# Kernel tuning notes

Measured on AMD Instinct MI355X. Metric: run time of the kernel, lower is better.

Reference implementation:

```python
import jax, jax.numpy as jnp
import numpy as np

NEG_INF = -9e15  # matches the torch source's large-negative mask value
LRELU_SLOPE = 0.2


def setup_inputs() -> dict:
    key = jax.random.key(0)
    k1, k2, k3, k4, k5, k6 = jax.random.split(key, 6)
    N, D_IN, D_OUT = 8192, 512, 256
    h = jax.random.normal(k1, (N, D_IN), dtype=jnp.float32)
    adj = jax.random.randint(k2, (N, N), 0, 2, dtype=jnp.int32)
    # xavier_uniform with gain=1.414 for W [out, in] and a [1, 2*out]
    lim_W = 1.414 * np.sqrt(6.0 / (D_IN + D_OUT))
    lim_a = 1.414 * np.sqrt(6.0 / (2 * D_OUT + 1))
    W_w = jax.random.uniform(k3, (D_OUT, D_IN), minval=-lim_W, maxval=lim_W, dtype=jnp.float32)
    W_b = jax.random.normal(k4, (D_OUT,), dtype=jnp.float32) * 0.01
    a_w = jax.random.uniform(k5, (1, 2 * D_OUT), minval=-lim_a, maxval=lim_a, dtype=jnp.float32)
    a_b = jax.random.normal(k6, (1,), dtype=jnp.float32) * 0.01
    return {"h": h, "adj": adj, "W_w": W_w, "W_b": W_b, "a_w": a_w, "a_b": a_b}


def reference(h, adj, W_w, W_b, a_w, a_b):
    # wh = W(h): [N, d_out]
    wh = h @ W_w.T + W_b
    d_out = wh.shape[-1]
    # a(cat([wh_i, wh_j])) decomposes: a_src . wh_i + a_dst . wh_j + a_b
    # (identical math to the O(N^2 * 2d) repeat/cat in the torch source)
    a_src, a_dst = a_w[0, :d_out], a_w[0, d_out:]
    s_src = wh @ a_src  # [N]
    s_dst = wh @ a_dst  # [N]
    e = jax.nn.leaky_relu(s_src[:, None] + s_dst[None, :] + a_b[0], LRELU_SLOPE)  # [N, N]
    masked = jnp.where(adj > 0, e, jnp.float32(NEG_INF))
    attn = jax.nn.softmax(masked, axis=1)  # softmax over neighbors j
    return attn @ wh  # [N, d_out]
```

## Files before the change

kernel.cpp:

```cpp
#include <hip/hip_runtime.h>

typedef unsigned short ushort_t;
typedef unsigned int uint_t;
typedef __attribute__((ext_vector_type(8))) short short8;
typedef __attribute__((ext_vector_type(4))) float f32x4;
typedef __attribute__((ext_vector_type(4))) int i32x4;
typedef __attribute__((ext_vector_type(4))) uint_t u32x4;
typedef __attribute__((ext_vector_type(4))) ushort_t u16x4;

#define LRELU_SLOPE 0.2f
#define LOG2E 1.44269504f

static __device__ __forceinline__ ushort_t f2bf(float f) {
    uint_t u = __builtin_bit_cast(uint_t, f);
    uint_t r = (u + 0x7fffu + ((u >> 16) & 1u)) >> 16;
    return (ushort_t)r;
}
static __device__ __forceinline__ uint4 pack8(float4 a, float4 b) {
    uint4 r;
    r.x = (uint_t)f2bf(a.x) | ((uint_t)f2bf(a.y) << 16);
    r.y = (uint_t)f2bf(a.z) | ((uint_t)f2bf(a.w) << 16);
    r.z = (uint_t)f2bf(b.x) | ((uint_t)f2bf(b.y) << 16);
    r.w = (uint_t)f2bf(b.z) | ((uint_t)f2bf(b.w) << 16);
    return r;
}
static __device__ __forceinline__ uint_t cvt_pk_bf16(float lo, float hi) {
    uint_t r;
    asm("v_cvt_pk_bf16_f32 %0, %1, %2" : "=v"(r) : "v"(lo), "v"(hi));
    return r;
}

__launch_bounds__(256, 2)
__global__ void k1_gemm(const float* __restrict__ h, const float* __restrict__ W,
                        const float* __restrict__ Wb, const float* __restrict__ aw,
                        ushort_t* __restrict__ whB, float* __restrict__ s_src,
                        float* __restrict__ s_dst) {
    __shared__ __align__(16) ushort_t aT[256 * 72];
    __shared__ __align__(16) ushort_t bT[32 * 72];
    __shared__ float redLds[2][4][32];

    const int t = threadIdx.x;
    const int wv = t >> 6, ln = t & 63;
    const int i0 = blockIdx.x * 32;
    const int srow = t >> 3, sch = t & 7;
    const int row0 = ln & 15, kq = ln >> 4;

    f32x4 acc[4][2];
#pragma unroll
    for (int mt = 0; mt < 4; ++mt)
#pragma unroll
        for (int nt = 0; nt < 2; ++nt) acc[mt][nt] = (f32x4){0.f, 0.f, 0.f, 0.f};

    for (int k0 = 0; k0 < 512; k0 += 64) {
        __syncthreads();
#pragma unroll
        for (int r = 0; r < 8; ++r) {
            const float* gp = W + (size_t)(r * 32 + srow) * 512 + k0 + sch * 8;
            float4 x0 = *(const float4*)gp;
            float4 x1 = *(const float4*)(gp + 4);
            *(uint4*)(aT + (r * 32 + srow) * 72 + sch * 8) = pack8(x0, x1);
        }
        {
            const float* gp = h + (size_t)(i0 + srow) * 512 + k0 + sch * 8;
            float4 x0 = *(const float4*)gp;
            float4 x1 = *(const float4*)(gp + 4);
            *(uint4*)(bT + srow * 72 + sch * 8) = pack8(x0, x1);
        }
        __syncthreads();
#pragma unroll
        for (int ks = 0; ks < 2; ++ks) {
            short8 b[2];
#pragma unroll
            for (int nt = 0; nt < 2; ++nt)
                b[nt] = *(const short8*)(bT + (nt * 16 + row0) * 72 + ks * 32 + kq * 8);
#pragma unroll
            for (int mt = 0; mt < 4; ++mt) {
                short8 a = *(const short8*)(aT + (wv * 64 + mt * 16 + row0) * 72 + ks * 32 + kq * 8);
#pragma unroll
                for (int nt = 0; nt < 2; ++nt)
                    acc[mt][nt] = __builtin_amdgcn_mfma_f32_16x16x32_bf16(a, b[nt], acc[mt][nt], 0, 0, 0);
            }
        }
    }

    float psrc[2] = {0.f, 0.f}, pdst[2] = {0.f, 0.f};
#pragma unroll
    for (int mt = 0; mt < 4; ++mt) {
#pragma unroll
        for (int r = 0; r < 4; ++r) {
            const int o = wv * 64 + mt * 16 + (ln >> 4) * 4 + r;
            const float wbv = Wb[o];
            const float as = aw[o];
            const float ad = aw[256 + o];
#pragma unroll
            for (int nt = 0; nt < 2; ++nt) {
                const float v = acc[mt][nt][r] + wbv;
                psrc[nt] += v * as;
                pdst[nt] += v * ad;
                const int i = i0 + nt * 16 + (ln & 15);
                const int jt = i >> 6;
                const int khi = (i >> 5) & 1;
                const int kqi = (i >> 3) & 3;
                whB[((size_t)(jt * 2 + khi) * 256 + o) * 32 + kqi * 8 + (i & 7)] = f2bf(v);
            }
        }
    }
#pragma unroll
    for (int off = 16; off < 64; off <<= 1) {
#pragma unroll
        for (int nt = 0; nt < 2; ++nt) {
            psrc[nt] += __shfl_xor(psrc[nt], off, 64);
            pdst[nt] += __shfl_xor(pdst[nt], off, 64);
        }
    }
    if (ln < 16) {
#pragma unroll
        for (int nt = 0; nt < 2; ++nt) {
            redLds[0][wv][nt * 16 + ln] = psrc[nt];
            redLds[1][wv][nt * 16 + ln] = pdst[nt];
        }
    }
    __syncthreads();
    if (t < 32) {
        float s = 0.f;
#pragma unroll
        for (int w = 0; w < 4; ++w) s += redLds[0][w][t];
        s_src[i0 + t] = s * LOG2E;
    } else if (t < 64) {
        float s = 0.f;
#pragma unroll
        for (int w = 0; w < 4; ++w) s += redLds[1][w][t - 32];
        s_dst[i0 + t - 32] = s * LOG2E;
    }
}

__launch_bounds__(512, 2)
__global__ void k2_attn(const int* __restrict__ adj, const ushort_t* __restrict__ whB,
                        const float* __restrict__ s_src, const float* __restrict__ s_dst,
                        const float* __restrict__ ab_p, float* __restrict__ out0,
                        float* __restrict__ out1, float* __restrict__ zp, int jsplit) {
    __shared__ __align__(16) char smem[66560 + 256];
    ushort_t* pbuf = (ushort_t*)smem;
    float* exch = (float*)smem;
    float* zLds = (float*)(smem + 66560);

    const int t = threadIdx.x;
    const int wv = t >> 6, ln = t & 63;
    const int dq = wv & 3, kh = wv >> 2;
    const int row0 = ln & 15, kq = ln >> 4;
    const int split2 = (jsplit == 2);
    const int jb = split2 ? (int)(blockIdx.x & 1) : 0;
    const int ib = split2 ? (int)(blockIdx.x >> 1) : (int)blockIdx.x;
    const int i0 = ib * 64;
    const int jlen = split2 ? 4096 : 8192;
    const int jbase = jb * jlen;
    const int iters = jlen >> 6;
    const int prow = t >> 4, pjc = t & 15;

    const float ab = ab_p[0] * LOG2E;
    const float ssa0 = s_src[i0 + prow] + ab;
    const float ssa1 = s_src[i0 + 32 + prow] + ab;

    const int* aBase0 = adj + (size_t)(i0 + prow) * 8192 + jbase + pjc * 4;
    const int* aBase1 = aBase0 + (size_t)32 * 8192;
    const float* sBase = s_dst + jbase + pjc * 4;
    const ushort_t* bBase = whB + ((size_t)(jbase >> 6) * 2 + kh) * 8192
                            + (dq * 64 + row0) * 32 + kq * 8;

    f32x4 acc[4][4];
#pragma unroll
    for (int mt = 0; mt < 4; ++mt)
#pragma unroll
        for (int nt = 0; nt < 4; ++nt) acc[mt][nt] = (f32x4){0.f, 0.f, 0.f, 0.f};
    float zacc0 = 0.f, zacc1 = 0.f;

    i32x4 Av0 = __builtin_nontemporal_load((const i32x4*)aBase0);
    i32x4 Av1 = __builtin_nontemporal_load((const i32x4*)aBase1);
    f32x4 Sv = *(const f32x4*)sBase;
    short8 Bv[4];
#pragma unroll
    for (int nt = 0; nt < 4; ++nt) Bv[nt] = *(const short8*)(bBase + nt * 512);

#pragma unroll 2
    for (int it = 0; it < iters; ++it) {
        const int itn = (it < iters - 1) ? it + 1 : it;
        i32x4 Ac0 = Av0, Ac1 = Av1;
        f32x4 Sc = Sv;
        short8 Bc[4];
#pragma unroll
        for (int nt = 0; nt < 4; ++nt) Bc[nt] = Bv[nt];
        Av0 = __builtin_nontemporal_load((const i32x4*)(aBase0 + itn * 64));
        Av1 = __builtin_nontemporal_load((const i32x4*)(aBase1 + itn * 64));
        Sv = *(const f32x4*)(sBase + itn * 64);
        {
            const ushort_t* bN = bBase + (size_t)itn * 16384;
#pragma unroll
            for (int nt = 0; nt < 4; ++nt) Bv[nt] = *(const short8*)(bN + nt * 512);
        }

        {
            ushort_t* pc = pbuf + (it & 1) * 4608;
            float p[4];
            float z4 = 0.f;
#pragma unroll
            for (int k = 0; k < 4; ++k) {
                float sc = ssa0 + Sc[k];
                sc = fmaxf(sc, LRELU_SLOPE * sc);
                sc = fminf(sc, 86.562f);
                float pv = (Ac0[k] > 0) ? __builtin_amdgcn_exp2f(sc) : 0.f;
                z4 += pv;
                p[k] = pv;
            }
            zacc0 += z4;
            uint2 w0;
            w0.x = cvt_pk_bf16(p[0], p[1]);
            w0.y = cvt_pk_bf16(p[2], p[3]);
            *(uint2*)(pc + prow * 72 + pjc * 4) = w0;
            z4 = 0.f;
#pragma unroll
            for (int k = 0; k < 4; ++k) {
                float sc = ssa1 + Sc[k];
                sc = fmaxf(sc, LRELU_SLOPE * sc);
                sc = fminf(sc, 86.562f);
                float pv = (Ac1[k] > 0) ? __builtin_amdgcn_exp2f(sc) : 0.f;
                z4 += pv;
                p[k] = pv;
            }
            zacc1 += z4;
            uint2 w1;
            w1.x = cvt_pk_bf16(p[0], p[1]);
            w1.y = cvt_pk_bf16(p[2], p[3]);
            *(uint2*)(pc + (32 + prow) * 72 + pjc * 4) = w1;
        }
        __syncthreads();
        {
            const ushort_t* pc = pbuf + (it & 1) * 4608;
#pragma unroll
            for (int mt = 0; mt < 4; ++mt) {
                short8 a = *(const short8*)(pc + (mt * 16 + row0) * 72 + kh * 32 + kq * 8);
#pragma unroll
                for (int nt = 0; nt < 4; ++nt)
                    acc[mt][nt] = __builtin_amdgcn_mfma_f32_16x16x32_bf16(a, Bc[nt], acc[mt][nt], 0, 0, 0);
            }
        }
    }

    zacc0 += __shfl_xor(zacc0, 1, 64);
    zacc1 += __shfl_xor(zacc1, 1, 64);
    zacc0 += __shfl_xor(zacc0, 2, 64);
    zacc1 += __shfl_xor(zacc1, 2, 64);
    zacc0 += __shfl_xor(zacc0, 4, 64);
    zacc1 += __shfl_xor(zacc1, 4, 64);
    zacc0 += __shfl_xor(zacc0, 8, 64);
    zacc1 += __shfl_xor(zacc1, 8, 64);
    if ((t & 15) == 0) {
        if (split2) {
            zp[(size_t)jb * 8192 + i0 + prow] = zacc0;
            zp[(size_t)jb * 8192 + i0 + 32 + prow] = zacc1;
        } else {
            zLds[prow] = 1.0f / fmaxf(zacc0, 1e-30f);
            zLds[32 + prow] = 1.0f / fmaxf(zacc1, 1e-30f);
        }
    }

    __syncthreads();
    if (kh == 1) {
        float* p = exch + (dq * 64 + ln) * 65;
#pragma unroll
        for (int mt = 0; mt < 4; ++mt)
#pragma unroll
            for (int nt = 0; nt < 4; ++nt)
#pragma unroll
                for (int r = 0; r < 4; ++r) p[mt * 16 + nt * 4 + r] = acc[mt][nt][r];
    }
    __syncthreads();
    if (kh == 0) {
        float* outp = (jb == 0) ? out0 : out1;
        const float* p = exch + (dq * 64 + ln) * 65;
#pragma unroll
        for (int mt = 0; mt < 4; ++mt)
#pragma unroll
            for (int nt = 0; nt < 4; ++nt)
#pragma unroll
                for (int r = 0; r < 4; ++r) {
                    const int il = mt * 16 + (ln >> 4) * 4 + r;
                    const int d = dq * 64 + nt * 16 + (ln & 15);
                    const float v = acc[mt][nt][r] + p[mt * 16 + nt * 4 + r];
                    if (split2)
                        outp[(size_t)(i0 + il) * 256 + d] = v;
                    else
                        outp[(size_t)(i0 + il) * 256 + d] = v * zLds[il];
                }
    }
}

__global__ void k3_norm(float* __restrict__ out, const float* __restrict__ part,
                        const float* __restrict__ zp) {
    const int i = blockIdx.x, t = threadIdx.x;
    const float rz = 1.0f / fmaxf(zp[i] + zp[8192 + i], 1e-30f);
    const size_t idx = (size_t)i * 256 + t;
    out[idx] = (out[idx] + part[idx]) * rz;
}

extern "C" void kernel_launch(void* const* d_in, const int* in_sizes, int n_in, void* d_out,
                              int out_size, void* d_ws, size_t ws_size, hipStream_t stream) {
    int order[16];
    for (int i = 0; i < n_in; ++i) order[i] = i;
    for (int a = 0; a < n_in; ++a)
        for (int b = a + 1; b < n_in; ++b)
            if (in_sizes[order[b]] < in_sizes[order[a]]) {
                int tmp = order[a]; order[a] = order[b]; order[b] = tmp;
            }
    const float* ab = (const float*)d_in[order[0]];
    const float* Wb = (const float*)d_in[order[1]];
    const float* aw = (const float*)d_in[order[2]];
    const float* Ww = (const float*)d_in[order[3]];
    const float* h = (const float*)d_in[order[4]];
    const int* adj = (const int*)d_in[order[5]];

    char* ws = (char*)d_ws;
    ushort_t* whB = (ushort_t*)ws;
    float* ssrc = (float*)(ws + 4194304);
    float* sdst = (float*)(ws + 4227072);
    float* part = (float*)(ws + 4259840);
    float* zp = (float*)(ws + 12648448);
    const size_t need = 12713984;
    const int jsplit = (ws_size >= need) ? 2 : 1;

    hipLaunchKernelGGL(k1_gemm, dim3(256), dim3(256), 0, stream, h, Ww, Wb, aw, whB, ssrc, sdst);
    hipLaunchKernelGGL(k2_attn, dim3(128 * jsplit), dim3(512), 0, stream, adj, whB, ssrc, sdst,
                       ab, (float*)d_out, part, zp, jsplit);
    if (jsplit == 2)
        hipLaunchKernelGGL(k3_norm, dim3(8192), dim3(256), 0, stream, (float*)d_out, part, zp);
}
```

Before: 420.1 us.

## Fuse split-K normalization into attention kernel via last-arriver atomic flag

Removes the separate k3_norm launch. Each of the two j-split blocks writes its partial output and row sums to workspace, then increments a per-row-tile atomic counter. The block that arrives second reads the other block's partial and writes the final normalized output. The counters are reset inside k1_gemm. Software bf16 rounding is also replaced with the hardware v_cvt_pk_bf16 instruction. The cost is a larger workspace, an extra round of partial writes and reads, and reliance on correct fence/atomic ordering.

```diff
diff --git a/kernel.cpp b/kernel.cpp
--- a/kernel.cpp
+++ b/kernel.cpp
@@ -11,30 +11,28 @@
 #define LRELU_SLOPE 0.2f
 #define LOG2E 1.44269504f
 
-static __device__ __forceinline__ ushort_t f2bf(float f) {
-    uint_t u = __builtin_bit_cast(uint_t, f);
-    uint_t r = (u + 0x7fffu + ((u >> 16) & 1u)) >> 16;
-    return (ushort_t)r;
-}
-static __device__ __forceinline__ uint4 pack8(float4 a, float4 b) {
-    uint4 r;
-    r.x = (uint_t)f2bf(a.x) | ((uint_t)f2bf(a.y) << 16);
-    r.y = (uint_t)f2bf(a.z) | ((uint_t)f2bf(a.w) << 16);
-    r.z = (uint_t)f2bf(b.x) | ((uint_t)f2bf(b.y) << 16);
-    r.w = (uint_t)f2bf(b.z) | ((uint_t)f2bf(b.w) << 16);
-    return r;
-}
 static __device__ __forceinline__ uint_t cvt_pk_bf16(float lo, float hi) {
     uint_t r;
     asm("v_cvt_pk_bf16_f32 %0, %1, %2" : "=v"(r) : "v"(lo), "v"(hi));
     return r;
 }
+static __device__ __forceinline__ ushort_t f2bf_hw(float f) {
+    return (ushort_t)(cvt_pk_bf16(f, f) & 0xffffu);
+}
+static __device__ __forceinline__ uint4 pack8(float4 a, float4 b) {
+    uint4 r;
+    r.x = cvt_pk_bf16(a.x, a.y);
+    r.y = cvt_pk_bf16(a.z, a.w);
+    r.z = cvt_pk_bf16(b.x, b.y);
+    r.w = cvt_pk_bf16(b.z, b.w);
+    return r;
+}
 
 __launch_bounds__(256, 2)
 __global__ void k1_gemm(const float* __restrict__ h, const float* __restrict__ W,
                         const float* __restrict__ Wb, const float* __restrict__ aw,
                         ushort_t* __restrict__ whB, float* __restrict__ s_src,
-                        float* __restrict__ s_dst) {
+                        float* __restrict__ s_dst, int* __restrict__ flags) {
     __shared__ __align__(16) ushort_t aT[256 * 72];
     __shared__ __align__(16) ushort_t bT[32 * 72];
     __shared__ float redLds[2][4][32];
@@ -44,6 +42,8 @@
     const int i0 = blockIdx.x * 32;
     const int srow = t >> 3, sch = t & 7;
     const int row0 = ln & 15, kq = ln >> 4;
+
+    if (t == 0 && blockIdx.x < 128) flags[blockIdx.x] = 0;
 
     f32x4 acc[4][2];
 #pragma unroll
@@ -101,7 +101,7 @@
                 const int jt = i >> 6;
                 const int khi = (i >> 5) & 1;
                 const int kqi = (i >> 3) & 3;
-                whB[((size_t)(jt * 2 + khi) * 256 + o) * 32 + kqi * 8 + (i & 7)] = f2bf(v);
+                whB[((size_t)(jt * 2 + khi) * 256 + o) * 32 + kqi * 8 + (i & 7)] = f2bf_hw(v);
             }
         }
     }
@@ -137,12 +137,14 @@
 __launch_bounds__(512, 2)
 __global__ void k2_attn(const int* __restrict__ adj, const ushort_t* __restrict__ whB,
                         const float* __restrict__ s_src, const float* __restrict__ s_dst,
-                        const float* __restrict__ ab_p, float* __restrict__ out0,
-                        float* __restrict__ out1, float* __restrict__ zp, int jsplit) {
-    __shared__ __align__(16) char smem[66560 + 256];
+                        const float* __restrict__ ab_p, float* __restrict__ out,
+                        float* __restrict__ part0, float* __restrict__ part1,
+                        float* __restrict__ zp, int* __restrict__ flags, int jsplit) {
+    __shared__ __align__(16) char smem[66560 + 256 + 16];
     ushort_t* pbuf = (ushort_t*)smem;
     float* exch = (float*)smem;
     float* zLds = (float*)(smem + 66560);
+    int* sflag = (int*)(smem + 66560 + 256);
 
     const int t = threadIdx.x;
     const int wv = t >> 6, ln = t & 63;
@@ -254,12 +256,11 @@
     zacc0 += __shfl_xor(zacc0, 8, 64);
     zacc1 += __shfl_xor(zacc1, 8, 64);
     if ((t & 15) == 0) {
+        zLds[prow] = zacc0;
+        zLds[32 + prow] = zacc1;
         if (split2) {
             zp[(size_t)jb * 8192 + i0 + prow] = zacc0;
             zp[(size_t)jb * 8192 + i0 + 32 + prow] = zacc1;
-        } else {
-            zLds[prow] = 1.0f / fmaxf(zacc0, 1e-30f);
-            zLds[32 + prow] = 1.0f / fmaxf(zacc1, 1e-30f);
         }
     }
 
@@ -275,31 +276,64 @@
     }
     __syncthreads();
     if (kh == 0) {
-        float* outp = (jb == 0) ? out0 : out1;
         const float* p = exch + (dq * 64 + ln) * 65;
-#pragma unroll
-        for (int mt = 0; mt < 4; ++mt)
-#pragma unroll
-            for (int nt = 0; nt < 4; ++nt)
-#pragma unroll
-                for (int r = 0; r < 4; ++r) {
-                    const int il = mt * 16 + (ln >> 4) * 4 + r;
-                    const int d = dq * 64 + nt * 16 + (ln & 15);
-                    const float v = acc[mt][nt][r] + p[mt * 16 + nt * 4 + r];
-                    if (split2)
-                        outp[(size_t)(i0 + il) * 256 + d] = v;
-                    else
-                        outp[(size_t)(i0 + il) * 256 + d] = v * zLds[il];
-                }
-    }
-}
-
-__global__ void k3_norm(float* __restrict__ out, const float* __restrict__ part,
-                        const float* __restrict__ zp) {
-    const int i = blockIdx.x, t = threadIdx.x;
-    const float rz = 1.0f / fmaxf(zp[i] + zp[8192 + i], 1e-30f);
-    const size_t idx = (size_t)i * 256 + t;
-    out[idx] = (out[idx] + part[idx]) * rz;
+        if (split2) {
+            float* myp = (jb == 0) ? part0 : part1;
+#pragma unroll
+            for (int mt = 0; mt < 4; ++mt)
+#pragma unroll
+                for (int nt = 0; nt < 4; ++nt)
+#pragma unroll
+                    for (int r = 0; r < 4; ++r) {
+                        const int il = mt * 16 + (ln >> 4) * 4 + r;
+                        const int d = dq * 64 + nt * 16 + (ln & 15);
+                        const float v = acc[mt][nt][r] + p[mt * 16 + nt * 4 + r];
+                        acc[mt][nt][r] = v;
+                        myp[(size_t)(i0 + il) * 256 + d] = v;
+                    }
+        } else {
+#pragma unroll
+            for (int mt = 0; mt < 4; ++mt)
+#pragma unroll
+                for (int nt = 0; nt < 4; ++nt)
+#pragma unroll
+                    for (int r = 0; r < 4; ++r) {
+                        const int il = mt * 16 + (ln >> 4) * 4 + r;
+                        const int d = dq * 64 + nt * 16 + (ln & 15);
+                        const float v = acc[mt][nt][r] + p[mt * 16 + nt * 4 + r];
+                        out[(size_t)(i0 + il) * 256 + d] = v / fmaxf(zLds[il], 1e-30f);
+                    }
+        }
+    }
+
+    if (split2) {
+        __threadfence();
+        __syncthreads();
+        if (t == 0)
+            *sflag = __hip_atomic_fetch_add(&flags[ib], 1, __ATOMIC_ACQ_REL,
+                                            __HIP_MEMORY_SCOPE_AGENT);
+        __syncthreads();
+        if (*sflag == 1) {
+            __threadfence();
+            if (kh == 0) {
+                const float* op = (jb == 0) ? part1 : part0;
+                const float* zo = zp + (size_t)(1 - jb) * 8192 + i0;
+#pragma unroll
+                for (int mt = 0; mt < 4; ++mt)
+#pragma unroll
+                    for (int r = 0; r < 4; ++r) {
+                        const int il = mt * 16 + (ln >> 4) * 4 + r;
+                        const float rz = 1.0f / fmaxf(zLds[il] + zo[il], 1e-30f);
+#pragma unroll
+                        for (int nt = 0; nt < 4; ++nt) {
+                            const int d = dq * 64 + nt * 16 + (ln & 15);
+                            const size_t idx = (size_t)(i0 + il) * 256 + d;
+                            out[idx] = (acc[mt][nt][r] + op[idx]) * rz;
+                        }
+                    }
+            }
+        }
+    }
 }
 
 extern "C" void kernel_launch(void* const* d_in, const int* in_sizes, int n_in, void* d_out,
@@ -322,14 +356,15 @@
     ushort_t* whB = (ushort_t*)ws;
     float* ssrc = (float*)(ws + 4194304);
     float* sdst = (float*)(ws + 4227072);
-    float* part = (float*)(ws + 4259840);
-    float* zp = (float*)(ws + 12648448);
-    const size_t need = 12713984;
+    float* part0 = (float*)(ws + 4259840);
+    float* part1 = (float*)(ws + 12648448);
+    float* zp = (float*)(ws + 21037056);
+    int* flags = (int*)(ws + 21102592);
+    const size_t need = 21103104;
     const int jsplit = (ws_size >= need) ? 2 : 1;
 
-    hipLaunchKernelGGL(k1_gemm, dim3(256), dim3(256), 0, stream, h, Ww, Wb, aw, whB, ssrc, sdst);
+    hipLaunchKernelGGL(k1_gemm, dim3(256), dim3(256), 0, stream, h, Ww, Wb, aw, whB, ssrc,
+                       sdst, flags);
     hipLaunchKernelGGL(k2_attn, dim3(128 * jsplit), dim3(512), 0, stream, adj, whB, ssrc, sdst,
-                       ab, (float*)d_out, part, zp, jsplit);
-    if (jsplit == 2)
-        hipLaunchKernelGGL(k3_norm, dim3(8192), dim3(256), 0, stream, (float*)d_out, part, zp);
-}
+                       ab, (float*)d_out, part0, part1, zp, flags, jsplit);
+}
```

Measured after the change: 527.3 us. +25.5%, slower.
